# Kernel optimization log

Measured on AMD Instinct MI355X. Metric: run time of the kernel, lower is better.

## Reference

```python
import jax, jax.numpy as jnp
import numpy as np

B, N, M, R, W, H, NIN, OUT = 32, 1024, 64, 4, 1, 512, 256, 256
RM = 1 + 2 * W  # read modes: backward(W), content(1), forward(W)
SIZES = [W*M, W*M, R, W, W, R*RM, W*M, W, R*M, R]
OFFS = np.cumsum([0] + SIZES)
P = int(OFFS[-1])
EPS = 1e-8


def setup_inputs():
    key = jax.random.key(0)
    ks = jax.random.split(key, 20)
    norm = lambda w: w / jnp.sum(w, axis=-1, keepdims=True)
    return {
        'X': jax.random.normal(ks[0], (B, NIN), jnp.float32),
        'backward_embeddings': jax.random.normal(ks[1], (B, H), jnp.float32),
        'memory': jax.random.normal(ks[2], (B, N, M), jnp.float32) * 0.1,
        'prev_read': jax.random.normal(ks[3], (B, R, M), jnp.float32) * 0.01,
        'h0': jax.random.normal(ks[4], (B, H), jnp.float32) * 0.1,
        'c0': jax.random.normal(ks[5], (B, H), jnp.float32) * 0.1,
        'read_w_prev': norm(jax.random.uniform(ks[6], (B, R, N), jnp.float32)),
        'write_w_prev': norm(jax.random.uniform(ks[7], (B, W, N), jnp.float32)),
        'usage_prev': jax.random.uniform(ks[8], (B, W, N), jnp.float32) * 0.5,
        'prec_prev': norm(jax.random.uniform(ks[9], (B, W, N), jnp.float32)),
        'links_prev': jnp.zeros((B, W, N, N), jnp.float32),
        'lstm_Wx': jax.random.normal(ks[10], (NIN + R * M, 4 * H), jnp.float32) * 0.02,
        'lstm_Wh': jax.random.normal(ks[11], (H, 4 * H), jnp.float32) * 0.02,
        'lstm_b': jnp.zeros((4 * H,), jnp.float32),
        'para_W': jax.random.normal(ks[12], (2 * H, P), jnp.float32) * 0.02,
        'para_b': jax.random.normal(ks[13], (P,), jnp.float32) * 0.01,
        'ln_g': jnp.ones((P,), jnp.float32),
        'ln_b': jnp.zeros((P,), jnp.float32),
        'proc_W': jax.random.normal(ks[14], (2 * H + R * M, OUT), jnp.float32) * 0.02,
        'proc_b': jnp.zeros((OUT,), jnp.float32),
    }


def _content(keys, beta, mem):
    # cosine-similarity content addressing: keys [B,h,M], beta [B,h], mem [B,N,M] -> [B,h,N]
    kn = keys / (jnp.linalg.norm(keys, axis=-1, keepdims=True) + EPS)
    mn = mem / (jnp.linalg.norm(mem, axis=-1, keepdims=True) + EPS)
    sim = jnp.einsum('bhm,bnm->bhn', kn, mn)
    return jax.nn.softmax(beta[..., None] * sim, axis=-1)


def _layernorm(x, g, b):
    mu = jnp.mean(x, axis=-1, keepdims=True)
    var = jnp.var(x, axis=-1, keepdims=True)
    return (x - mu) / jnp.sqrt(var + 1e-5) * g + b


def reference(X, backward_embeddings, memory, prev_read, h0, c0,
              read_w_prev, write_w_prev, usage_prev, prec_prev, links_prev,
              lstm_Wx, lstm_Wh, lstm_b, para_W, para_b, ln_g, ln_b, proc_W, proc_b):
    # ---- controller (single LSTM step) ----
    inp = jnp.concatenate([X, prev_read.reshape(B, R * M)], axis=1)
    gates = inp @ lstm_Wx + h0 @ lstm_Wh + lstm_b
    i, f, g, o = jnp.split(gates, 4, axis=1)
    c = jax.nn.sigmoid(f) * c0 + jax.nn.sigmoid(i) * jnp.tanh(g)
    h = jax.nn.sigmoid(o) * jnp.tanh(c)  # c_output [B,H]

    # ---- param_operations ----
    pvec = _layernorm(jnp.concatenate([h, backward_embeddings], axis=1) @ para_W + para_b, ln_g, ln_b)
    sl = lambda k: pvec[:, OFFS[k]:OFFS[k + 1]]
    write_vectors = sl(0).reshape(B, W, M)
    erase_vectors = jax.nn.sigmoid(sl(1)).reshape(B, W, M)
    free_gate = jax.nn.sigmoid(sl(2))                      # [B,R]
    alloc_gate = jax.nn.sigmoid(sl(3))                     # [B,W]
    write_gate = jax.nn.sigmoid(sl(4))                     # [B,W]
    read_mode = jax.nn.softmax(sl(5).reshape(B, R, RM), axis=2)
    write_keys = sl(6).reshape(B, W, M)
    write_strengths = 1.0 + jax.nn.softplus(sl(7))         # [B,W]
    read_keys = sl(8).reshape(B, R, M)
    read_strengths = 1.0 + jax.nn.softplus(sl(9))          # [B,R]

    # ---- usage + allocation ----
    psi = jnp.prod(1.0 - free_gate[:, :, None] * read_w_prev, axis=1)          # [B,N]
    usage = (usage_prev + write_w_prev - usage_prev * write_w_prev) * psi[:, None, :]  # [B,W,N]
    order = jnp.argsort(usage, axis=-1)
    u_sorted = jnp.take_along_axis(usage, order, axis=-1)
    vals = (1.0 - u_sorted) * jnp.cumprod(u_sorted, axis=-1)  # inclusive cumprod (as in source)
    inv = jnp.argsort(order, axis=-1)
    alloc = jnp.take_along_axis(vals, inv, axis=-1)           # [B,W,N]

    # ---- write weights ----
    wc = _content(write_keys, write_strengths, memory)        # [B,W,N]
    ww = write_gate[..., None] * (alloc_gate[..., None] * alloc + (1.0 - alloc_gate[..., None]) * wc)

    # ---- memory write (sequential over write heads) ----
    mem = memory
    for wi in range(W):
        w = ww[:, wi]                                         # [B,N]
        mem = mem * (1.0 - w[:, :, None] * erase_vectors[:, wi, None, :]) \
              + w[:, :, None] * write_vectors[:, wi, None, :]

    # ---- temporal links ----
    eye = jnp.eye(N, dtype=mem.dtype)
    new_links, new_prec = [], []
    for wi in range(W):
        w = ww[:, wi]
        p = prec_prev[:, wi]
        L = links_prev[:, wi]
        Lnew = (1.0 - w[:, :, None] - w[:, None, :]) * L + w[:, :, None] * p[:, None, :]
        Lnew = Lnew * (1.0 - eye)                             # zero diagonal
        new_links.append(Lnew)
        new_prec.append((1.0 - jnp.sum(w, axis=1, keepdims=True)) * p + w)
    links = jnp.stack(new_links, axis=1)                      # [B,W,N,N]

    # ---- read weights: backward(W) | content | forward(W) ----
    rc = _content(read_keys, read_strengths, mem)             # [B,R,N]
    fwd = jnp.einsum('bwij,brj->bwri', links, read_w_prev)    # L @ w_prev
    bwd = jnp.einsum('bwji,brj->bwri', links, read_w_prev)    # L^T @ w_prev
    rw = read_mode[:, :, W][..., None] * rc
    for wi in range(W):
        rw = rw + read_mode[:, :, wi][..., None] * bwd[:, wi] \
                + read_mode[:, :, W + 1 + wi][..., None] * fwd[:, wi]

    # ---- reads + output projection ----
    reads = jnp.einsum('brn,bnm->brm', rw, mem)               # [B,R,M]
    out = jnp.concatenate([h, backward_embeddings, reads.reshape(B, R * M)], axis=1) @ proc_W + proc_b
    return out
```

## Files before the change

kernel.cpp:

```cpp
#include <hip/hip_runtime.h>
#include <math.h>

#define Bb 32
#define Nn 1024
#define Mm 64
#define Rr 4
#define Hh 512
#define NINq 256
#define Pp 471
#define EPSN 1e-8f

__device__ __forceinline__ float sigm(float x){ return 1.0f/(1.0f+expf(-x)); }

__global__ __launch_bounds__(256) void k_gates(
    const float* __restrict__ X, const float* __restrict__ pr,
    const float* __restrict__ h0, const float* __restrict__ Wx,
    const float* __restrict__ Wh, float* __restrict__ gpart)
{
  __shared__ float lin[32][64];
  int tid = threadIdx.x;
  int col = blockIdx.x*64 + (tid & 63);
  int bg  = tid >> 6;
  int k0  = blockIdx.y*64;
#pragma unroll
  for (int q=0;q<8;q++){
    int idx = tid + 256*q;
    int bb = idx >> 6, kk = idx & 63;
    int k = k0 + kk;
    float v;
    if (k < 256)      v = X [bb*NINq + k];
    else if (k < 512) v = pr[bb*(Rr*Mm) + (k-256)];
    else              v = h0[bb*Hh + (k-512)];
    lin[bb][kk] = v;
  }
  __syncthreads();
  const float* Wr = (k0 < 512) ? (Wx + (size_t)k0*2048)
                               : (Wh + (size_t)(k0-512)*2048);
  float acc[8];
#pragma unroll
  for (int i=0;i<8;i++) acc[i]=0.f;
#pragma unroll 8
  for (int kk=0; kk<64; ++kk){
    float wv = Wr[(size_t)kk*2048 + col];
#pragma unroll
    for (int bb=0; bb<8; ++bb) acc[bb] += wv * lin[bg*8+bb][kk];
  }
  float* gp = gpart + (size_t)blockIdx.y*65536;
#pragma unroll
  for (int bb=0; bb<8; ++bb)
    gp[(bg*8+bb)*2048 + col] = acc[bb];
}

__global__ void k_lstm_ep(const float* __restrict__ gpart, const float* __restrict__ lb,
                          const float* __restrict__ c0, const float* __restrict__ emb,
                          float* __restrict__ hcat, float* __restrict__ ocat)
{
  int idx = blockIdx.x*blockDim.x + threadIdx.x;
  if (idx >= Bb*Hh) return;
  int b = idx >> 9, j = idx & 511;
  float gi = lb[j], gf = lb[j+512], gg = lb[j+1024], go = lb[j+1536];
  for (int c=0;c<16;++c){
    const float* gp = gpart + (size_t)c*65536 + b*2048;
    gi += gp[j]; gf += gp[j+512]; gg += gp[j+1024]; go += gp[j+1536];
  }
  float c = sigm(gf)*c0[idx] + sigm(gi)*tanhf(gg);
  float h = sigm(go)*tanhf(c);
  float e = emb[idx];
  hcat[b*1024 + j]       = h;
  hcat[b*1024 + 512 + j] = e;
  ocat[b*1280 + j]       = h;
  ocat[b*1280 + 512 + j] = e;
}

__global__ __launch_bounds__(256) void k_para(
    const float* __restrict__ hcat, const float* __restrict__ Wp,
    float* __restrict__ ppart)
{
  __shared__ float lin[32][64];
  int tid = threadIdx.x;
  int col = blockIdx.x*64 + (tid & 63);
  int bg  = tid >> 6;
  int k0  = blockIdx.y*64;
#pragma unroll
  for (int q=0;q<8;q++){
    int idx = tid + 256*q;
    int bb = idx >> 6, kk = idx & 63;
    lin[bb][kk] = hcat[bb*1024 + k0 + kk];
  }
  __syncthreads();
  int colc = (col < Pp) ? col : (Pp-1);
  const float* Wr = Wp + (size_t)k0*Pp;
  float acc[8];
#pragma unroll
  for (int i=0;i<8;i++) acc[i]=0.f;
#pragma unroll 8
  for (int kk=0; kk<64; ++kk){
    float wv = Wr[(size_t)kk*Pp + colc];
#pragma unroll
    for (int bb=0; bb<8; ++bb) acc[bb] += wv * lin[bg*8+bb][kk];
  }
  if (col < Pp) {
    float* pp = ppart + (size_t)blockIdx.y*16384;
#pragma unroll
    for (int bb=0; bb<8; ++bb)
      pp[(bg*8+bb)*512 + col] = acc[bb];
  }
}

__global__ __launch_bounds__(1024) void k_waddr(
    const float* __restrict__ ppart, const float* __restrict__ bp,
    const float* __restrict__ ln_g, const float* __restrict__ ln_b,
    const float* __restrict__ rwp, const float* __restrict__ wwp,
    const float* __restrict__ up, const float* __restrict__ mem,
    const float* __restrict__ prec,
    float* __restrict__ pvec, float* __restrict__ wwb, float* __restrict__ spsw)
{
  __shared__ float red[16];
  __shared__ float pvs[512];
  __shared__ float fg[4];
  __shared__ float kdir[64];
  __shared__ float scal[4];
  __shared__ unsigned long long sk[1024];
  __shared__ float wsums[16];
  __shared__ float af[1024];
  __shared__ float red8[16][8];
  int b = blockIdx.x, tid = threadIdx.x;
  int lane = tid & 63, wv = tid >> 6;
  float acc = 0.f, d = 0.f;
  if (tid < 512) {
    if (tid < Pp) {
      acc = bp[tid];
#pragma unroll
      for (int c=0;c<16;++c) acc += ppart[(size_t)c*16384 + b*512 + tid];
    }
    float s = acc;
    for (int o=32;o;o>>=1) s += __shfl_xor(s,o,64);
    if (lane==0) red[wv] = s;
  }
  __syncthreads();
  if (tid < 8){ float xx = red[tid]; for (int o=4;o;o>>=1) xx += __shfl_xor(xx,o,64); if (!tid) red[0]=xx; }
  __syncthreads();
  float mu = red[0] / (float)Pp;
  __syncthreads();
  if (tid < 512) {
    d = (tid < Pp) ? (acc - mu) : 0.f;
    float s2 = d*d;
    for (int o=32;o;o>>=1) s2 += __shfl_xor(s2,o,64);
    if (lane==0) red[wv] = s2;
  }
  __syncthreads();
  if (tid < 8){ float xx = red[tid]; for (int o=4;o;o>>=1) xx += __shfl_xor(xx,o,64); if (!tid) red[0]=xx; }
  __syncthreads();
  float var = red[0] / (float)Pp;
  if (tid < Pp) {
    float y = d / sqrtf(var + 1e-5f) * ln_g[tid] + ln_b[tid];
    pvec[b*512 + tid] = y;
    pvs[tid] = y;
  }
  __syncthreads();
  if (tid < 4) fg[tid] = sigm(pvs[128+tid]);
  if (wv == 0) {
    float v = pvs[146 + lane];
    float s = v*v;
    for (int o=32;o;o>>=1) s += __shfl_xor(s,o,64);
    kdir[lane] = v / (sqrtf(s) + EPSN);
  }
  if (tid == 0) {
    scal[0] = sigm(pvs[132]);
    scal[1] = sigm(pvs[133]);
    scal[2] = 1.f + log1pf(expf(pvs[210]));
  }
  __syncthreads();
  float psi = 1.f;
#pragma unroll
  for (int r=0;r<4;r++) psi *= 1.f - fg[r]*rwp[b*(Rr*Nn) + r*Nn + tid];
  float u = up[b*Nn+tid], w = wwp[b*Nn+tid];
  float usage = (u + w - u*w)*psi;
  unsigned long long key = ((unsigned long long)__float_as_uint(usage) << 32) | (unsigned)tid;
  for (int k=2; k<=1024; k<<=1) {
    for (int j=k>>1; j>0; j>>=1) {
      bool lower = (tid & j) == 0;
      bool asc   = (tid & k) == 0;
      unsigned long long pk;
      if (j >= 64) {
        sk[tid] = key; __syncthreads();
        pk = sk[tid ^ j];
        __syncthreads();
      } else {
        pk = __shfl_xor(key, j, 64);
      }
      key = ((key < pk) == (lower == asc)) ? key : pk;
    }
  }
  float us = __uint_as_float((unsigned)(key >> 32));
  int order = (int)(key & 1023u);
  float v = us;
#pragma unroll
  for (int dd=1; dd<64; dd<<=1) {
    float p = __shfl_up(v, dd, 64);
    if (lane >= dd) v *= p;
  }
  if (lane == 63) wsums[wv] = v;
  __syncthreads();
  if (wv == 0) {
    float t = (lane < 16) ? wsums[lane] : 1.f;
#pragma unroll
    for (int dd=1; dd<16; dd<<=1) {
      float p = __shfl_up(t, dd, 64);
      if (lane >= dd) t *= p;
    }
    if (lane < 16) wsums[lane] = t;
  }
  __syncthreads();
  float prefix = (wv > 0) ? wsums[wv-1] : 1.f;
  af[order] = (1.f - us) * (v * prefix);
  float beta = scal[2];
  float dot = 0.f, s2 = 0.f;
  const float* mrow = mem + (size_t)(b*Nn + tid)*Mm;
#pragma unroll
  for (int j=0;j<16;j++){
    float4 mv = *reinterpret_cast<const float4*>(&mrow[j*4]);
    dot += mv.x*kdir[j*4] + mv.y*kdir[j*4+1] + mv.z*kdir[j*4+2] + mv.w*kdir[j*4+3];
    s2  += mv.x*mv.x + mv.y*mv.y + mv.z*mv.z + mv.w*mv.w;
  }
  float sim = beta * dot / (sqrtf(s2) + EPSN);
  float m_ = sim;
  for (int o=32;o;o>>=1) m_ = fmaxf(m_, __shfl_xor(m_,o,64));
  if (lane==0) red[wv] = m_;
  __syncthreads();
  if (tid < 16){ float x = red[tid]; for (int o=8;o;o>>=1) x = fmaxf(x,__shfl_xor(x,o,64)); if (!tid) red[0]=x; }
  __syncthreads();
  float gmax = red[0];
  __syncthreads();
  float e = expf(sim - gmax);
  float ss = e;
  for (int o=32;o;o>>=1) ss += __shfl_xor(ss,o,64);
  if (lane==0) red[wv] = ss;
  __syncthreads();
  if (tid < 16){ float x = red[tid]; for (int o=8;o;o>>=1) x += __shfl_xor(x,o,64); if (!tid) red[0]=x; }
  __syncthreads();
  float wcn = e / red[0];
  float ag = scal[0], wg = scal[1];
  float wwn = wg * (ag*af[tid] + (1.f-ag)*wcn);
  wwb[b*Nn + tid] = wwn;
  float p = prec[b*Nn + tid];
#pragma unroll
  for (int r=0;r<4;r++){
    float a = rwp[b*(Rr*Nn) + r*Nn + tid];
    float x1 = p*a, x2 = wwn*a;
    for (int o=32;o;o>>=1){ x1 += __shfl_xor(x1,o,64); x2 += __shfl_xor(x2,o,64); }
    if (lane==0){ red8[wv][r] = x1; red8[wv][4+r] = x2; }
  }
  __syncthreads();
  if (tid < 8) {
    float s = 0.f;
    for (int w2=0; w2<16; ++w2) s += red8[w2][tid];
    spsw[b*8 + tid] = s;
  }
}

__global__ __launch_bounds__(256) void k_linksmem(
    const float* __restrict__ links, const float* __restrict__ rwp,
    const float* __restrict__ wwb, const float* __restrict__ pvec,
    const float* __restrict__ mem,
    float* __restrict__ S1p, float* __restrict__ S2p,
    float* __restrict__ T1p, float* __restrict__ T2p,
    float* __restrict__ diag, float* __restrict__ memn, float* __restrict__ simr)
{
  int b = blockIdx.y;
  int tid = threadIdx.x;
  if (blockIdx.x >= 32) {
    __shared__ float ev[64], wvv[64];
    __shared__ float kdir4[4][64];
    __shared__ float beta4[4];
    int stripe = blockIdx.x - 32;
    int wv = tid>>6, lane = tid&63;
    const float* pv = pvec + b*512;
    {
      float kv = pv[211 + wv*64 + lane];
      float s = kv*kv;
      for (int o=32;o;o>>=1) s += __shfl_xor(s,o,64);
      kdir4[wv][lane] = kv/(sqrtf(s)+EPSN);
      if (lane==0) beta4[wv] = 1.f + log1pf(expf(pv[467+wv]));
    }
    if (tid < 64) { wvv[tid] = pv[tid]; ev[tid] = sigm(pv[64+tid]); }
    __syncthreads();
    for (int t=0;t<16;++t){
      int n = stripe*64 + wv*16 + t;
      float wwn = wwb[b*Nn + n];
      float v = mem[(b*Nn+n)*Mm + lane];
      float nv = v*(1.f - wwn*ev[lane]) + wwn*wvv[lane];
      memn[(b*Nn+n)*Mm + lane] = nv;
      float s2 = nv*nv;
      float d0 = nv*kdir4[0][lane], d1 = nv*kdir4[1][lane];
      float d2 = nv*kdir4[2][lane], d3 = nv*kdir4[3][lane];
      for (int o=32;o;o>>=1){
        s2 += __shfl_xor(s2,o,64);
        d0 += __shfl_xor(d0,o,64); d1 += __shfl_xor(d1,o,64);
        d2 += __shfl_xor(d2,o,64); d3 += __shfl_xor(d3,o,64);
      }
      if (lane==0){
        float inv = 1.f/(sqrtf(s2)+EPSN);
        simr[(b*4+0)*Nn+n] = beta4[0]*d0*inv;
        simr[(b*4+1)*Nn+n] = beta4[1]*d1*inv;
        simr[(b*4+2)*Nn+n] = beta4[2]*d2*inv;
        simr[(b*4+3)*Nn+n] = beta4[3]*d3*inv;
      }
    }
    return;
  }
  __shared__ float tile[64][65];
  __shared__ float ai[4][64], wai[4][64], aj[4][64], waj[4][64];
  int stripe = blockIdx.x >> 1, half = blockIdx.x & 1;
  int i0 = stripe*64, jbase = half*512;
  {
    int r = tid>>6, ii = tid&63;
    float a = rwp[b*(Rr*Nn) + r*Nn + i0+ii];
    ai[r][ii]  = a;
    wai[r][ii] = a * wwb[b*Nn + i0+ii];
  }
  float s1a[4]={0,0,0,0}, s2a[4]={0,0,0,0};
  const float* Lb = links + (size_t)b*Nn*Nn;
  const int lrow = tid>>4, c4 = tid&15;
  float4 pv[4];
#pragma unroll
  for (int q=0;q<4;q++)
    pv[q] = *reinterpret_cast<const float4*>(&Lb[(size_t)(i0+lrow+16*q)*Nn + jbase + c4*4]);
  const int dt = (half == (stripe>>3)) ? (stripe&7) : -1;
  for (int t=0; t<8; ++t) {
    int j0 = jbase + t*64;
    __syncthreads();
#pragma unroll
    for (int q=0;q<4;q++){
      int row = lrow + 16*q;
      float4 v = pv[q];
      tile[row][c4*4+0]=v.x; tile[row][c4*4+1]=v.y;
      tile[row][c4*4+2]=v.z; tile[row][c4*4+3]=v.w;
    }
    {
      int r = tid>>6, jj = tid&63;
      float a = rwp[b*(Rr*Nn) + r*Nn + j0+jj];
      aj[r][jj]  = a;
      waj[r][jj] = a * wwb[b*Nn + j0+jj];
    }
    __syncthreads();
    if (t < 7) {
      int j0n = j0 + 64;
#pragma unroll
      for (int q=0;q<4;q++)
        pv[q] = *reinterpret_cast<const float4*>(&Lb[(size_t)(i0+lrow+16*q)*Nn + j0n + c4*4]);
    }
    if (t == dt && tid < 64) diag[b*Nn + i0 + tid] = tile[tid][tid];
    {
      int ii = tid>>2, c = tid&3;
      float p1[4]={0,0,0,0}, p2[4]={0,0,0,0};
      for (int k=0;k<16;k++){
        int jj = c*16+k;
        float v = tile[ii][jj];
#pragma unroll
        for (int r=0;r<4;r++){ p1[r] += v*aj[r][jj]; p2[r] += v*waj[r][jj]; }
      }
#pragma unroll
      for (int r=0;r<4;r++){
        p1[r] += __shfl_xor(p1[r],1,64); p1[r] += __shfl_xor(p1[r],2,64);
        p2[r] += __shfl_xor(p2[r],1,64); p2[r] += __shfl_xor(p2[r],2,64);
      }
      if (c==0){
#pragma unroll
        for (int r=0;r<4;r++){ s1a[r] += p1[r]; s2a[r] += p2[r]; }
      }
    }
    {
      int jj = tid>>2, q = tid&3;
      float p1[4]={0,0,0,0}, p2[4]={0,0,0,0};
      for (int k=0;k<16;k++){
        int ii = q*16+k;
        float v = tile[ii][jj];
#pragma unroll
        for (int r=0;r<4;r++){ p1[r] += v*ai[r][ii]; p2[r] += v*wai[r][ii]; }
      }
#pragma unroll
      for (int r=0;r<4;r++){
        p1[r] += __shfl_xor(p1[r],1,64); p1[r] += __shfl_xor(p1[r],2,64);
        p2[r] += __shfl_xor(p2[r],1,64); p2[r] += __shfl_xor(p2[r],2,64);
      }
      if (q==0){
#pragma unroll
        for (int r=0;r<4;r++){
          size_t o = (size_t)(((b*4+r)*16 + stripe))*Nn + j0 + jj;
          T1p[o] = p1[r];
          T2p[o] = p2[r];
        }
      }
    }
  }
  if ((tid&3)==0){
    int ii = tid>>2;
#pragma unroll
    for (int r=0;r<4;r++){
      size_t o = (size_t)(((half*Bb + b)*4 + r))*Nn + i0 + ii;
      S1p[o] = s1a[r];
      S2p[o] = s2a[r];
    }
  }
}

__global__ __launch_bounds__(1024) void k_rread(
    const float* __restrict__ pvec, const float* __restrict__ rwp,
    const float* __restrict__ prec, const float* __restrict__ wwb,
    const float* __restrict__ T1p, const float* __restrict__ T2p,
    const float* __restrict__ S1p, const float* __restrict__ S2p,
    const float* __restrict__ spsw, const float* __restrict__ diag,
    const float* __restrict__ simr, const float* __restrict__ memn,
    const float* __restrict__ bo, float* __restrict__ ocat, float* __restrict__ out)
{
  __shared__ float rwl[4][1024];
  __shared__ float red[16];
  __shared__ float rm3s[4][3];
  __shared__ float rp[16][4][64];
  int b = blockIdx.x, tid = threadIdx.x;
  int wv = tid>>6, lane = tid&63;
  const float* pv = pvec + b*512;
  if (tid < 4) {
    float x0 = pv[134+tid*3], x1 = pv[134+tid*3+1], x2 = pv[134+tid*3+2];
    float mx = fmaxf(x0, fmaxf(x1,x2));
    float e0 = expf(x0-mx), e1 = expf(x1-mx), e2 = expf(x2-mx);
    float s = e0+e1+e2;
    rm3s[tid][0]=e0/s; rm3s[tid][1]=e1/s; rm3s[tid][2]=e2/s;
  }
  float w_n = wwb[b*Nn + tid];
  float p_n = prec[b*Nn + tid];
  float Lii = diag[b*Nn + tid];
  __syncthreads();
  for (int r=0;r<4;++r){
    float v = simr[(b*4+r)*Nn + tid];
    float m_ = v;
    for (int o=32;o;o>>=1) m_ = fmaxf(m_, __shfl_xor(m_,o,64));
    if (lane==0) red[wv]=m_;
    __syncthreads();
    if (tid<16){ float x=red[tid]; for(int o=8;o;o>>=1) x=fmaxf(x,__shfl_xor(x,o,64)); if(!tid) red[0]=x; }
    __syncthreads();
    float gmax = red[0];
    __syncthreads();
    float e = expf(v-gmax);
    float s = e;
    for (int o=32;o;o>>=1) s += __shfl_xor(s,o,64);
    if (lane==0) red[wv]=s;
    __syncthreads();
    if (tid<16){ float x=red[tid]; for(int o=8;o;o>>=1) x+=__shfl_xor(x,o,64); if(!tid) red[0]=x; }
    __syncthreads();
    float rc = e/red[0];
    float s1v = S1p[(size_t)((0*Bb+b)*4+r)*Nn + tid] + S1p[(size_t)((1*Bb+b)*4+r)*Nn + tid];
    float s2v = S2p[(size_t)((0*Bb+b)*4+r)*Nn + tid] + S2p[(size_t)((1*Bb+b)*4+r)*Nn + tid];
    float t1v = 0.f, t2v = 0.f;
#pragma unroll
    for (int st=0; st<16; ++st){
      size_t o = (size_t)((b*4+r)*16 + st)*Nn + tid;
      t1v += T1p[o];
      t2v += T2p[o];
    }
    float a = rwp[b*(Rr*Nn)+r*Nn+tid];
    float Spr = spsw[b*8+r], Swr = spsw[b*8+4+r];
    float fwd = (1.f-w_n)*(s1v - Lii*a) - (s2v - Lii*w_n*a) + w_n*(Spr - p_n*a);
    float bwd = (1.f-w_n)*(t1v - Lii*a) - (t2v - w_n*Lii*a) + p_n*(Swr - w_n*a);
    rwl[r][tid] = rm3s[r][1]*rc + rm3s[r][0]*bwd + rm3s[r][2]*fwd;
    __syncthreads();
  }
  float a0=0.f, a1=0.f, a2=0.f, a3=0.f;
  for (int t=0;t<64;++t){
    int n = wv*64 + t;
    float v = memn[(size_t)(b*Nn+n)*Mm + lane];
    a0 += rwl[0][n]*v; a1 += rwl[1][n]*v; a2 += rwl[2][n]*v; a3 += rwl[3][n]*v;
  }
  rp[wv][0][lane]=a0; rp[wv][1][lane]=a1; rp[wv][2][lane]=a2; rp[wv][3][lane]=a3;
  __syncthreads();
  if (tid < 256) {
    int r = tid>>6, m = tid&63;
    float s = 0.f;
#pragma unroll
    for (int w2=0;w2<16;++w2) s += rp[w2][r][m];
    ocat[b*1280 + 1024 + r*64 + m] = s;
    out[b*256 + tid] = bo[tid];
  }
}

__global__ __launch_bounds__(256) void k_gout(
    const float* __restrict__ ocat, const float* __restrict__ Wo,
    float* __restrict__ out)
{
  __shared__ float lin[32][64];
  int tid = threadIdx.x;
  int col = blockIdx.x*64 + (tid & 63);
  int bg  = tid >> 6;
  int k0  = blockIdx.y*64;
#pragma unroll
  for (int q=0;q<8;q++){
    int idx = tid + 256*q;
    int bb = idx >> 6, kk = idx & 63;
    lin[bb][kk] = ocat[bb*1280 + k0 + kk];
  }
  __syncthreads();
  const float* Wr = Wo + (size_t)k0*256;
  float acc[8];
#pragma unroll
  for (int i=0;i<8;i++) acc[i]=0.f;
#pragma unroll 8
  for (int kk=0; kk<64; ++kk){
    float wv = Wr[(size_t)kk*256 + col];
#pragma unroll
    for (int bb=0; bb<8; ++bb) acc[bb] += wv * lin[bg*8+bb][kk];
  }
#pragma unroll
  for (int bb=0; bb<8; ++bb)
    atomicAdd(&out[(size_t)(bg*8+bb)*256 + col], acc[bb]);
}

extern "C" void kernel_launch(void* const* d_in, const int* in_sizes, int n_in,
                              void* d_out, int out_size, void* d_ws, size_t ws_size,
                              hipStream_t stream)
{
  (void)in_sizes; (void)n_in; (void)out_size; (void)ws_size;
  const float* X    = (const float*)d_in[0];
  const float* emb  = (const float*)d_in[1];
  const float* mem  = (const float*)d_in[2];
  const float* prvr = (const float*)d_in[3];
  const float* h0   = (const float*)d_in[4];
  const float* c0   = (const float*)d_in[5];
  const float* rwp  = (const float*)d_in[6];
  const float* wwp  = (const float*)d_in[7];
  const float* up   = (const float*)d_in[8];
  const float* prec = (const float*)d_in[9];
  const float* links= (const float*)d_in[10];
  const float* Wx   = (const float*)d_in[11];
  const float* Wh   = (const float*)d_in[12];
  const float* lb   = (const float*)d_in[13];
  const float* Wp   = (const float*)d_in[14];
  const float* bp   = (const float*)d_in[15];
  const float* lng  = (const float*)d_in[16];
  const float* lnb  = (const float*)d_in[17];
  const float* Wo   = (const float*)d_in[18];
  const float* bo   = (const float*)d_in[19];
  float* out = (float*)d_out;
  float* ws  = (float*)d_ws;

  float* memn  = ws;
  float* T1p   = memn  + 2097152;
  float* T2p   = T1p   + 2097152;
  float* S1p   = T2p   + 2097152;
  float* S2p   = S1p   + 262144;
  float* gpart = S2p   + 262144;
  float* ppart = gpart + 1048576;
  float* pvec  = ppart + 262144;
  float* wwb   = pvec  + 16384;
  float* ocat  = wwb   + 32768;
  float* spsw  = ocat  + 40960;
  float* simr  = spsw  + 256;
  float* diag  = simr  + 131072;
  float* hcat  = diag  + 32768;

  k_gates   <<<dim3(32,16), dim3(256),  0, stream>>>(X, prvr, h0, Wx, Wh, gpart);
  k_lstm_ep <<<dim3(64),    dim3(256),  0, stream>>>(gpart, lb, c0, emb, hcat, ocat);
  k_para    <<<dim3(8,16),  dim3(256),  0, stream>>>(hcat, Wp, ppart);
  k_waddr   <<<dim3(32),    dim3(1024), 0, stream>>>(ppart, bp, lng, lnb, rwp, wwp, up,
                                                     mem, prec, pvec, wwb, spsw);
  k_linksmem<<<dim3(48,32), dim3(256),  0, stream>>>(links, rwp, wwb, pvec, mem,
                                                     S1p, S2p, T1p, T2p, diag, memn, simr);
  k_rread   <<<dim3(32),    dim3(1024), 0, stream>>>(pvec, rwp, prec, wwb, T1p, T2p,
                                                     S1p, S2p, spsw, diag, simr, memn,
                                                     bo, ocat, out);
  k_gout    <<<dim3(4,20),  dim3(256),  0, stream>>>(ocat, Wo, out);
}
```

Measured before the change: 133.0 us.

## Enlarge link tiles to 128 rows and parallelize read-head softmax across thread groups

The link-matrix kernel now gives each block 128 rows instead of 64. This halves the number of partial column sums (T1p/T2p) written and then reduced in the read kernel, and the link-processing blocks shrink from 32 to 16 per batch. Shared memory is merged into one union buffer used by both block roles. The read kernel now runs the four heads' softmax and weight combination at the same time in four 256-thread groups instead of looping with many barriers, at the cost of fewer blocks for latency hiding and more registers per thread.

```diff
diff --git a/kernel.cpp b/kernel.cpp
--- a/kernel.cpp
+++ b/kernel.cpp
@@ -267,20 +267,22 @@
     float* __restrict__ T1p, float* __restrict__ T2p,
     float* __restrict__ diag, float* __restrict__ memn, float* __restrict__ simr)
 {
+  __shared__ float sm[9856];
   int b = blockIdx.y;
   int tid = threadIdx.x;
-  if (blockIdx.x >= 32) {
-    __shared__ float ev[64], wvv[64];
-    __shared__ float kdir4[4][64];
-    __shared__ float beta4[4];
-    int stripe = blockIdx.x - 32;
+  if (blockIdx.x >= 16) {
+    float* ev    = sm;
+    float* wvv   = sm + 64;
+    float* kdir4 = sm + 128;
+    float* beta4 = sm + 384;
+    int stripe = blockIdx.x - 16;
     int wv = tid>>6, lane = tid&63;
     const float* pv = pvec + b*512;
     {
       float kv = pv[211 + wv*64 + lane];
       float s = kv*kv;
       for (int o=32;o;o>>=1) s += __shfl_xor(s,o,64);
-      kdir4[wv][lane] = kv/(sqrtf(s)+EPSN);
+      kdir4[wv*64+lane] = kv/(sqrtf(s)+EPSN);
       if (lane==0) beta4[wv] = 1.f + log1pf(expf(pv[467+wv]));
     }
     if (tid < 64) { wvv[tid] = pv[tid]; ev[tid] = sigm(pv[64+tid]); }
@@ -292,8 +294,8 @@
       float nv = v*(1.f - wwn*ev[lane]) + wwn*wvv[lane];
       memn[(b*Nn+n)*Mm + lane] = nv;
       float s2 = nv*nv;
-      float d0 = nv*kdir4[0][lane], d1 = nv*kdir4[1][lane];
-      float d2 = nv*kdir4[2][lane], d3 = nv*kdir4[3][lane];
+      float d0 = nv*kdir4[0*64+lane], d1 = nv*kdir4[1*64+lane];
+      float d2 = nv*kdir4[2*64+lane], d3 = nv*kdir4[3*64+lane];
       for (int o=32;o;o>>=1){
         s2 += __shfl_xor(s2,o,64);
         d0 += __shfl_xor(d0,o,64); d1 += __shfl_xor(d1,o,64);
@@ -309,56 +311,66 @@
     }
     return;
   }
-  __shared__ float tile[64][65];
-  __shared__ float ai[4][64], wai[4][64], aj[4][64], waj[4][64];
-  int stripe = blockIdx.x >> 1, half = blockIdx.x & 1;
-  int i0 = stripe*64, jbase = half*512;
-  {
-    int r = tid>>6, ii = tid&63;
+  float (*tile)[65] = (float(*)[65])sm;
+  float* ai  = sm + 8320;
+  float* wai = sm + 8832;
+  float* aj  = sm + 9344;
+  float* waj = sm + 9600;
+  int sg = blockIdx.x >> 1, half = blockIdx.x & 1;
+  int i0 = sg*128, jbase = half*512;
+#pragma unroll
+  for (int e=0;e<2;++e){
+    int idx = tid + 256*e;
+    int r = idx>>7, ii = idx&127;
     float a = rwp[b*(Rr*Nn) + r*Nn + i0+ii];
-    ai[r][ii]  = a;
-    wai[r][ii] = a * wwb[b*Nn + i0+ii];
-  }
-  float s1a[4]={0,0,0,0}, s2a[4]={0,0,0,0};
+    ai[r*128+ii]  = a;
+    wai[r*128+ii] = a * wwb[b*Nn + i0+ii];
+  }
+  float s1a[2][4] = {{0,0,0,0},{0,0,0,0}}, s2a[2][4] = {{0,0,0,0},{0,0,0,0}};
   const float* Lb = links + (size_t)b*Nn*Nn;
   const int lrow = tid>>4, c4 = tid&15;
-  float4 pv[4];
-#pragma unroll
-  for (int q=0;q<4;q++)
-    pv[q] = *reinterpret_cast<const float4*>(&Lb[(size_t)(i0+lrow+16*q)*Nn + jbase + c4*4]);
-  const int dt = (half == (stripe>>3)) ? (stripe&7) : -1;
+  float4 pv4[8];
+#pragma unroll
+  for (int q=0;q<8;q++)
+    pv4[q] = *reinterpret_cast<const float4*>(&Lb[(size_t)(i0+lrow+16*q)*Nn + jbase + c4*4]);
   for (int t=0; t<8; ++t) {
     int j0 = jbase + t*64;
     __syncthreads();
 #pragma unroll
-    for (int q=0;q<4;q++){
+    for (int q=0;q<8;q++){
       int row = lrow + 16*q;
-      float4 v = pv[q];
+      float4 v = pv4[q];
       tile[row][c4*4+0]=v.x; tile[row][c4*4+1]=v.y;
       tile[row][c4*4+2]=v.z; tile[row][c4*4+3]=v.w;
     }
     {
       int r = tid>>6, jj = tid&63;
       float a = rwp[b*(Rr*Nn) + r*Nn + j0+jj];
-      aj[r][jj]  = a;
-      waj[r][jj] = a * wwb[b*Nn + j0+jj];
+      aj[r*64+jj]  = a;
+      waj[r*64+jj] = a * wwb[b*Nn + j0+jj];
     }
     __syncthreads();
     if (t < 7) {
       int j0n = j0 + 64;
 #pragma unroll
-      for (int q=0;q<4;q++)
-        pv[q] = *reinterpret_cast<const float4*>(&Lb[(size_t)(i0+lrow+16*q)*Nn + j0n + c4*4]);
-    }
-    if (t == dt && tid < 64) diag[b*Nn + i0 + tid] = tile[tid][tid];
-    {
-      int ii = tid>>2, c = tid&3;
+      for (int q=0;q<8;q++)
+        pv4[q] = *reinterpret_cast<const float4*>(&Lb[(size_t)(i0+lrow+16*q)*Nn + j0n + c4*4]);
+    }
+    int rowblock = half*8 + t;
+    if ((rowblock>>1) == sg && tid < 64) {
+      int lr0 = (rowblock&1)*64;
+      diag[b*Nn + rowblock*64 + tid] = tile[lr0+tid][tid];
+    }
+#pragma unroll
+    for (int h=0;h<2;++h){
+      int ii = h*64 + (tid>>2);
+      int c = tid&3;
       float p1[4]={0,0,0,0}, p2[4]={0,0,0,0};
       for (int k=0;k<16;k++){
         int jj = c*16+k;
         float v = tile[ii][jj];
 #pragma unroll
-        for (int r=0;r<4;r++){ p1[r] += v*aj[r][jj]; p2[r] += v*waj[r][jj]; }
+        for (int r=0;r<4;r++){ p1[r] += v*aj[r*64+jj]; p2[r] += v*waj[r*64+jj]; }
       }
 #pragma unroll
       for (int r=0;r<4;r++){
@@ -367,17 +379,17 @@
       }
       if (c==0){
 #pragma unroll
-        for (int r=0;r<4;r++){ s1a[r] += p1[r]; s2a[r] += p2[r]; }
+        for (int r=0;r<4;r++){ s1a[h][r] += p1[r]; s2a[h][r] += p2[r]; }
       }
     }
     {
       int jj = tid>>2, q = tid&3;
       float p1[4]={0,0,0,0}, p2[4]={0,0,0,0};
-      for (int k=0;k<16;k++){
-        int ii = q*16+k;
+      for (int k=0;k<32;k++){
+        int ii = q*32+k;
         float v = tile[ii][jj];
 #pragma unroll
-        for (int r=0;r<4;r++){ p1[r] += v*ai[r][ii]; p2[r] += v*wai[r][ii]; }
+        for (int r=0;r<4;r++){ p1[r] += v*ai[r*128+ii]; p2[r] += v*wai[r*128+ii]; }
       }
 #pragma unroll
       for (int r=0;r<4;r++){
@@ -387,7 +399,7 @@
       if (q==0){
 #pragma unroll
         for (int r=0;r<4;r++){
-          size_t o = (size_t)(((b*4+r)*16 + stripe))*Nn + j0 + jj;
+          size_t o = (size_t)((b*4+r)*8 + sg)*Nn + j0 + jj;
           T1p[o] = p1[r];
           T2p[o] = p2[r];
         }
@@ -397,10 +409,13 @@
   if ((tid&3)==0){
     int ii = tid>>2;
 #pragma unroll
-    for (int r=0;r<4;r++){
-      size_t o = (size_t)(((half*Bb + b)*4 + r))*Nn + i0 + ii;
-      S1p[o] = s1a[r];
-      S2p[o] = s2a[r];
+    for (int h=0;h<2;++h){
+#pragma unroll
+      for (int r=0;r<4;r++){
+        size_t o = (size_t)(((half*Bb + b)*4 + r))*Nn + i0 + h*64 + ii;
+        S1p[o] = s1a[h][r];
+        S2p[o] = s2a[h][r];
+      }
     }
   }
 }
@@ -415,11 +430,12 @@
     const float* __restrict__ bo, float* __restrict__ ocat, float* __restrict__ out)
 {
   __shared__ float rwl[4][1024];
-  __shared__ float red[16];
+  __shared__ float redm[4][4], reds[4][4];
   __shared__ float rm3s[4][3];
   __shared__ float rp[16][4][64];
   int b = blockIdx.x, tid = threadIdx.x;
-  int wv = tid>>6, lane = tid&63;
+  int g = tid>>8, t256 = tid&255;
+  int wv4 = (tid>>6)&3, lane = tid&63;
   const float* pv = pvec + b*512;
   if (tid < 4) {
     float x0 = pv[134+tid*3], x1 = pv[134+tid*3+1], x2 = pv[134+tid*3+2];
@@ -428,49 +444,51 @@
     float s = e0+e1+e2;
     rm3s[tid][0]=e0/s; rm3s[tid][1]=e1/s; rm3s[tid][2]=e2/s;
   }
-  float w_n = wwb[b*Nn + tid];
-  float p_n = prec[b*Nn + tid];
-  float Lii = diag[b*Nn + tid];
-  __syncthreads();
-  for (int r=0;r<4;++r){
-    float v = simr[(b*4+r)*Nn + tid];
-    float m_ = v;
-    for (int o=32;o;o>>=1) m_ = fmaxf(m_, __shfl_xor(m_,o,64));
-    if (lane==0) red[wv]=m_;
-    __syncthreads();
-    if (tid<16){ float x=red[tid]; for(int o=8;o;o>>=1) x=fmaxf(x,__shfl_xor(x,o,64)); if(!tid) red[0]=x; }
-    __syncthreads();
-    float gmax = red[0];
-    __syncthreads();
-    float e = expf(v-gmax);
-    float s = e;
-    for (int o=32;o;o>>=1) s += __shfl_xor(s,o,64);
-    if (lane==0) red[wv]=s;
-    __syncthreads();
-    if (tid<16){ float x=red[tid]; for(int o=8;o;o>>=1) x+=__shfl_xor(x,o,64); if(!tid) red[0]=x; }
-    __syncthreads();
-    float rc = e/red[0];
-    float s1v = S1p[(size_t)((0*Bb+b)*4+r)*Nn + tid] + S1p[(size_t)((1*Bb+b)*4+r)*Nn + tid];
-    float s2v = S2p[(size_t)((0*Bb+b)*4+r)*Nn + tid] + S2p[(size_t)((1*Bb+b)*4+r)*Nn + tid];
+  float v[4];
+#pragma unroll
+  for (int q=0;q<4;q++) v[q] = simr[(b*4+g)*Nn + t256 + 256*q];
+  float m_ = fmaxf(fmaxf(v[0],v[1]), fmaxf(v[2],v[3]));
+  for (int o=32;o;o>>=1) m_ = fmaxf(m_, __shfl_xor(m_,o,64));
+  if (lane==0) redm[g][wv4] = m_;
+  __syncthreads();
+  float gmax = fmaxf(fmaxf(redm[g][0],redm[g][1]), fmaxf(redm[g][2],redm[g][3]));
+  float e[4];
+  float ss = 0.f;
+#pragma unroll
+  for (int q=0;q<4;q++){ e[q] = expf(v[q]-gmax); ss += e[q]; }
+  for (int o=32;o;o>>=1) ss += __shfl_xor(ss,o,64);
+  if (lane==0) reds[g][wv4] = ss;
+  __syncthreads();
+  float tot = reds[g][0]+reds[g][1]+reds[g][2]+reds[g][3];
+  float Spr = spsw[b*8+g], Swr = spsw[b*8+4+g];
+#pragma unroll
+  for (int q=0;q<4;q++){
+    int n = t256 + 256*q;
+    float rc = e[q]/tot;
+    float w_n = wwb[b*Nn + n];
+    float p_n = prec[b*Nn + n];
+    float Lii = diag[b*Nn + n];
+    float a = rwp[b*(Rr*Nn)+g*Nn+n];
+    float s1v = S1p[(size_t)((0*Bb+b)*4+g)*Nn + n] + S1p[(size_t)((1*Bb+b)*4+g)*Nn + n];
+    float s2v = S2p[(size_t)((0*Bb+b)*4+g)*Nn + n] + S2p[(size_t)((1*Bb+b)*4+g)*Nn + n];
     float t1v = 0.f, t2v = 0.f;
 #pragma unroll
-    for (int st=0; st<16; ++st){
-      size_t o = (size_t)((b*4+r)*16 + st)*Nn + tid;
+    for (int st=0; st<8; ++st){
+      size_t o = (size_t)((b*4+g)*8 + st)*Nn + n;
       t1v += T1p[o];
       t2v += T2p[o];
     }
-    float a = rwp[b*(Rr*Nn)+r*Nn+tid];
-    float Spr = spsw[b*8+r], Swr = spsw[b*8+4+r];
     float fwd = (1.f-w_n)*(s1v - Lii*a) - (s2v - Lii*w_n*a) + w_n*(Spr - p_n*a);
     float bwd = (1.f-w_n)*(t1v - Lii*a) - (t2v - w_n*Lii*a) + p_n*(Swr - w_n*a);
-    rwl[r][tid] = rm3s[r][1]*rc + rm3s[r][0]*bwd + rm3s[r][2]*fwd;
-    __syncthreads();
-  }
+    rwl[g][n] = rm3s[g][1]*rc + rm3s[g][0]*bwd + rm3s[g][2]*fwd;
+  }
+  __syncthreads();
+  int wv = tid>>6;
   float a0=0.f, a1=0.f, a2=0.f, a3=0.f;
   for (int t=0;t<64;++t){
     int n = wv*64 + t;
-    float v = memn[(size_t)(b*Nn+n)*Mm + lane];
-    a0 += rwl[0][n]*v; a1 += rwl[1][n]*v; a2 += rwl[2][n]*v; a3 += rwl[3][n]*v;
+    float mv = memn[(size_t)(b*Nn+n)*Mm + lane];
+    a0 += rwl[0][n]*mv; a1 += rwl[1][n]*mv; a2 += rwl[2][n]*mv; a3 += rwl[3][n]*mv;
   }
   rp[wv][0][lane]=a0; rp[wv][1][lane]=a1; rp[wv][2][lane]=a2; rp[wv][3][lane]=a3;
   __syncthreads();
@@ -545,8 +563,8 @@
 
   float* memn  = ws;
   float* T1p   = memn  + 2097152;
-  float* T2p   = T1p   + 2097152;
-  float* S1p   = T2p   + 2097152;
+  float* T2p   = T1p   + 1048576;
+  float* S1p   = T2p   + 1048576;
   float* S2p   = S1p   + 262144;
   float* gpart = S2p   + 262144;
   float* ppart = gpart + 1048576;
@@ -563,7 +581,7 @@
   k_para    <<<dim3(8,16),  dim3(256),  0, stream>>>(hcat, Wp, ppart);
   k_waddr   <<<dim3(32),    dim3(1024), 0, stream>>>(ppart, bp, lng, lnb, rwp, wwp, up,
                                                      mem, prec, pvec, wwb, spsw);
-  k_linksmem<<<dim3(48,32), dim3(256),  0, stream>>>(links, rwp, wwb, pvec, mem,
+  k_linksmem<<<dim3(32,32), dim3(256),  0, stream>>>(links, rwp, wwb, pvec, mem,
                                                      S1p, S2p, T1p, T2p, diag, memn, simr);
   k_rread   <<<dim3(32),    dim3(1024), 0, stream>>>(pvec, rwp, prec, wwb, T1p, T2p,
                                                      S1p, S2p, spsw, diag, simr, memn,
```

Result: slower. 164.3 us (+23.6%).
